# Kernel optimization log

Measured on AMD Instinct MI355X. Metric: run time of the kernel, lower is better.

## Reference

```python
import jax, jax.numpy as jnp
import numpy as np

D_MODEL = 1024
NUM_HEADS = 16
HEAD_DIM = D_MODEL // NUM_HEADS
FFN_HIDDEN = 4096
EPS = 1e-5


def setup_inputs() -> dict:
    key = jax.random.key(0)
    ks = jax.random.split(key, 7)
    s = 0.02
    return {
        "x": jax.random.normal(ks[0], (2, 2048, D_MODEL), dtype=jnp.float32),
        "W_qkv": jax.random.normal(ks[1], (D_MODEL, 3 * D_MODEL), dtype=jnp.float32) * s,
        "b_qkv": jnp.zeros((3 * D_MODEL,), dtype=jnp.float32),
        "W_o": jax.random.normal(ks[2], (D_MODEL, D_MODEL), dtype=jnp.float32) * s,
        "b_o": jnp.zeros((D_MODEL,), dtype=jnp.float32),
        "gamma1": jnp.ones((D_MODEL,), dtype=jnp.float32),
        "beta1": jnp.zeros((D_MODEL,), dtype=jnp.float32),
        "W1": jax.random.normal(ks[3], (D_MODEL, FFN_HIDDEN), dtype=jnp.float32) * s,
        "b1": jnp.zeros((FFN_HIDDEN,), dtype=jnp.float32),
        "W2": jax.random.normal(ks[4], (FFN_HIDDEN, D_MODEL), dtype=jnp.float32) * s,
        "b2": jnp.zeros((D_MODEL,), dtype=jnp.float32),
        "gamma2": jnp.ones((D_MODEL,), dtype=jnp.float32),
        "beta2": jnp.zeros((D_MODEL,), dtype=jnp.float32),
    }


def _layernorm(x, gamma, beta):
    mean = jnp.mean(x, axis=-1, keepdims=True)
    var = jnp.mean((x - mean) ** 2, axis=-1, keepdims=True)
    return gamma * (x - mean) / jnp.sqrt(var + EPS) + beta


def reference(x, W_qkv, b_qkv, W_o, b_o, gamma1, beta1, W1, b1, W2, b2, gamma2, beta2):
    B, S, D = x.shape
    # ---- multi-head attention ----
    qkv = x @ W_qkv + b_qkv                       # [B,S,3D]
    qkv = qkv.reshape(B, S, NUM_HEADS, 3 * HEAD_DIM).transpose(0, 2, 1, 3)  # [B,H,S,3hd]
    q, k, v = jnp.split(qkv, 3, axis=-1)          # each [B,H,S,hd]
    scores = jnp.einsum("bhqd,bhkd->bhqk", q, k) / np.sqrt(HEAD_DIM)
    attn = jax.nn.softmax(scores, axis=-1)
    vals = jnp.einsum("bhqk,bhkd->bhqd", attn, v)
    vals = vals.transpose(0, 2, 1, 3).reshape(B, S, D)
    attn_out = vals @ W_o + b_o
    # dropout disabled (eval mode)
    h = _layernorm(attn_out + x, gamma1, beta1)
    # ---- position-wise FFN (dropout before relu per source, disabled) ----
    ffn = jax.nn.relu(h @ W1 + b1) @ W2 + b2
    return _layernorm(ffn + h, gamma2, beta2)
```

## Files before the change

### kernel.cpp

```cpp
#include <hip/hip_runtime.h>
#include <stdint.h>

typedef float v4f __attribute__((ext_vector_type(4)));
typedef __bf16 v8bf __attribute__((ext_vector_type(8)));
typedef unsigned short v8us __attribute__((ext_vector_type(8)));
typedef unsigned short v4us __attribute__((ext_vector_type(4)));

__device__ __forceinline__ float b2f(unsigned short u) {
    union { float f; uint32_t i; } x; x.i = ((uint32_t)u) << 16; return x.f;
}
__device__ __forceinline__ unsigned short f2b(float f) {
    union { float f; uint32_t u; } x; x.f = f;
    uint32_t r = x.u + 0x7fffu + ((x.u >> 16) & 1u);
    return (unsigned short)(r >> 16);
}

__device__ __forceinline__ void stage16(const unsigned short* g,
                                        unsigned short* lds_base, int lane) {
#if __has_builtin(__builtin_amdgcn_global_load_lds)
    __builtin_amdgcn_global_load_lds(
        (const __attribute__((address_space(1))) void*)g,
        (__attribute__((address_space(3))) void*)lds_base, 16, 0, 0);
#else
    *(v8us*)(lds_base + lane * 8) = *(const v8us*)g;
#endif
}

__global__ __launch_bounds__(256) void convert_f32_bf16(
    const float* __restrict__ src, unsigned short* __restrict__ dst)
{
    int i = (blockIdx.x * 256 + threadIdx.x) * 4;
    float4 v = *(const float4*)&src[i];
    v4us o = {f2b(v.x), f2b(v.y), f2b(v.z), f2b(v.w)};
    *(v4us*)&dst[i] = o;
}

__global__ __launch_bounds__(256) void transpose_to_bt(
    const float* __restrict__ W, unsigned short* __restrict__ WT, int K, int N)
{
    __shared__ unsigned short t[64][65];
    const int kb = blockIdx.y * 64, nb = blockIdx.x * 64;
    const int r = threadIdx.x >> 4, c4 = (threadIdx.x & 15) * 4;
    #pragma unroll
    for (int i = 0; i < 4; ++i) {
        int k = r + i * 16;
        float4 v = *(const float4*)&W[(size_t)(kb + k) * N + nb + c4];
        t[c4 + 0][k] = f2b(v.x);
        t[c4 + 1][k] = f2b(v.y);
        t[c4 + 2][k] = f2b(v.z);
        t[c4 + 3][k] = f2b(v.w);
    }
    __syncthreads();
    #pragma unroll
    for (int i = 0; i < 4; ++i) {
        int n = r + i * 16;
        v4us o = {t[n][c4], t[n][c4 + 1], t[n][c4 + 2], t[n][c4 + 3]};
        *(v4us*)&WT[(size_t)(nb + n) * K + kb + c4] = o;
    }
}

__global__ __launch_bounds__(256) void gemm_bt(
    const unsigned short* __restrict__ A, const unsigned short* __restrict__ BT,
    const float* __restrict__ bias, unsigned short* __restrict__ C,
    int M, int N, int K, int relu)
{
    __shared__ __align__(16) unsigned short sA[2][128 * 32];
    __shared__ __align__(16) unsigned short sB[2][128 * 32];
    const int tid  = threadIdx.x;
    const int wave = tid >> 6, lane = tid & 63;
    const int wm = wave >> 1, wn = wave & 1;
    const int quad = lane >> 4, l16 = lane & 15;
    const int bm = blockIdx.y, bn = blockIdx.x;

    const int srow = lane >> 2, scol = (lane & 3) * 8;
    const unsigned short* ga0 = A  + (size_t)(bm * 128 + (wave * 2 + 0) * 16 + srow) * K + scol;
    const unsigned short* ga1 = A  + (size_t)(bm * 128 + (wave * 2 + 1) * 16 + srow) * K + scol;
    const unsigned short* gb0 = BT + (size_t)(bn * 128 + (wave * 2 + 0) * 16 + srow) * K + scol;
    const unsigned short* gb1 = BT + (size_t)(bn * 128 + (wave * 2 + 1) * 16 + srow) * K + scol;
    const int o0 = (wave * 2 + 0) * 512, o1 = (wave * 2 + 1) * 512;

    v4f acc[4][4];
    #pragma unroll
    for (int i = 0; i < 4; ++i)
        #pragma unroll
        for (int j = 0; j < 4; ++j)
            acc[i][j] = (v4f){0.f, 0.f, 0.f, 0.f};

    for (int kt = 0; kt < K; kt += 64) {
        __syncthreads();
        #pragma unroll
        for (int c = 0; c < 2; ++c) {
            int kc = kt + c * 32;
            stage16(ga0 + kc, &sA[c][o0], lane);
            stage16(ga1 + kc, &sA[c][o1], lane);
            stage16(gb0 + kc, &sB[c][o0], lane);
            stage16(gb1 + kc, &sB[c][o1], lane);
        }
        __syncthreads();

        #pragma unroll
        for (int c = 0; c < 2; ++c) {
            v8bf af[4], bfr[4];
            #pragma unroll
            for (int mt = 0; mt < 4; ++mt)
                af[mt] = *(const v8bf*)&sA[c][(wm * 64 + mt * 16 + l16) * 32 + quad * 8];
            #pragma unroll
            for (int nt = 0; nt < 4; ++nt)
                bfr[nt] = *(const v8bf*)&sB[c][(wn * 64 + nt * 16 + l16) * 32 + quad * 8];
            #pragma unroll
            for (int mt = 0; mt < 4; ++mt)
                #pragma unroll
                for (int nt = 0; nt < 4; ++nt)
                    acc[mt][nt] = __builtin_amdgcn_mfma_f32_16x16x32_bf16(
                        af[mt], bfr[nt], acc[mt][nt], 0, 0, 0);
        }
    }

    #pragma unroll
    for (int mt = 0; mt < 4; ++mt) {
        #pragma unroll
        for (int nt = 0; nt < 4; ++nt) {
            int col = bn * 128 + wn * 64 + nt * 16 + l16;
            float bv = bias ? bias[col] : 0.f;
            #pragma unroll
            for (int r = 0; r < 4; ++r) {
                int row = bm * 128 + wm * 64 + mt * 16 + quad * 4 + r;
                float v = acc[mt][nt][r] + bv;
                if (relu) v = fmaxf(v, 0.f);
                C[(size_t)row * N + col] = f2b(v);
            }
        }
    }
}

__global__ __launch_bounds__(256) void gemm_bt_n64(
    const unsigned short* __restrict__ A, const unsigned short* __restrict__ BT,
    const float* __restrict__ bias, unsigned short* __restrict__ C,
    int M, int N, int K, int relu)
{
    __shared__ __align__(16) unsigned short sA[2][128 * 32];
    __shared__ __align__(16) unsigned short sB[2][64 * 32];
    const int tid  = threadIdx.x;
    const int wave = tid >> 6, lane = tid & 63;
    const int wm = wave >> 1, wn = wave & 1;
    const int quad = lane >> 4, l16 = lane & 15;
    const int bm = blockIdx.y, bn = blockIdx.x;

    const int srow = lane >> 2, scol = (lane & 3) * 8;
    const unsigned short* ga0 = A  + (size_t)(bm * 128 + (wave * 2 + 0) * 16 + srow) * K + scol;
    const unsigned short* ga1 = A  + (size_t)(bm * 128 + (wave * 2 + 1) * 16 + srow) * K + scol;
    const unsigned short* gb0 = BT + (size_t)(bn * 64 + wave * 16 + srow) * K + scol;
    const int oa0 = (wave * 2 + 0) * 512, oa1 = (wave * 2 + 1) * 512, ob = wave * 512;

    v4f acc[4][2];
    #pragma unroll
    for (int i = 0; i < 4; ++i)
        #pragma unroll
        for (int j = 0; j < 2; ++j)
            acc[i][j] = (v4f){0.f, 0.f, 0.f, 0.f};

    for (int kt = 0; kt < K; kt += 64) {
        __syncthreads();
        #pragma unroll
        for (int c = 0; c < 2; ++c) {
            int kc = kt + c * 32;
            stage16(ga0 + kc, &sA[c][oa0], lane);
            stage16(ga1 + kc, &sA[c][oa1], lane);
            stage16(gb0 + kc, &sB[c][ob], lane);
        }
        __syncthreads();

        #pragma unroll
        for (int c = 0; c < 2; ++c) {
            v8bf af[4], bfr[2];
            #pragma unroll
            for (int mt = 0; mt < 4; ++mt)
                af[mt] = *(const v8bf*)&sA[c][(wm * 64 + mt * 16 + l16) * 32 + quad * 8];
            #pragma unroll
            for (int nt = 0; nt < 2; ++nt)
                bfr[nt] = *(const v8bf*)&sB[c][(wn * 32 + nt * 16 + l16) * 32 + quad * 8];
            #pragma unroll
            for (int mt = 0; mt < 4; ++mt)
                #pragma unroll
                for (int nt = 0; nt < 2; ++nt)
                    acc[mt][nt] = __builtin_amdgcn_mfma_f32_16x16x32_bf16(
                        af[mt], bfr[nt], acc[mt][nt], 0, 0, 0);
        }
    }

    #pragma unroll
    for (int mt = 0; mt < 4; ++mt) {
        #pragma unroll
        for (int nt = 0; nt < 2; ++nt) {
            int col = bn * 64 + wn * 32 + nt * 16 + l16;
            float bv = bias ? bias[col] : 0.f;
            #pragma unroll
            for (int r = 0; r < 4; ++r) {
                int row = bm * 128 + wm * 64 + mt * 16 + quad * 4 + r;
                float v = acc[mt][nt][r] + bv;
                if (relu) v = fmaxf(v, 0.f);
                C[(size_t)row * N + col] = f2b(v);
            }
        }
    }
}

__global__ __launch_bounds__(256, 4) void attn_mfma(
    const unsigned short* __restrict__ qkv, unsigned short* __restrict__ av)
{
    __shared__ __align__(16) unsigned short sK[64 * 72];
    __shared__ __align__(16) unsigned short sVT[64 * 72];
    __shared__ __align__(16) unsigned short sP[4][16 * 72];
    const int tid  = threadIdx.x;
    const int wave = tid >> 6, lane = tid & 63;
    const int quad = lane >> 4, l16 = lane & 15;
    const int blk = blockIdx.x;
    const int qb = blk & 31, bh = blk >> 5;
    const int h = bh & 15, b = bh >> 4;
    const int row0 = b * 2048;
    const int qbase = row0 + qb * 64 + wave * 16;
    const size_t qoff = (size_t)h * 192;
    const size_t koff = qoff + 64, voff = qoff + 128;

    v8bf qf[2];
    #pragma unroll
    for (int kc = 0; kc < 2; ++kc)
        qf[kc] = *(const v8bf*)&qkv[(size_t)(qbase + l16) * 3072 + qoff + kc * 32 + quad * 8];

    v4f o[4];
    #pragma unroll
    for (int dt = 0; dt < 4; ++dt) o[dt] = (v4f){0.f, 0.f, 0.f, 0.f};
    float ll = 0.f;

    const float C1 = 0.125f * 1.44269504089f;

    const int k_key0 = tid >> 3,        k_oct = (tid & 7) * 8;
    const int k_key1 = (tid + 256) >> 3;
    const int v_key  = tid & 63;
    const int v_d0   = (tid >> 6) * 8,  v_d1 = v_d0 + 32;
    const unsigned short* gK0 = qkv + (size_t)(row0 + k_key0) * 3072 + koff + k_oct;
    const unsigned short* gK1 = qkv + (size_t)(row0 + k_key1) * 3072 + koff + k_oct;
    const unsigned short* gV0 = qkv + (size_t)(row0 + v_key) * 3072 + voff + v_d0;
    const unsigned short* gV1 = qkv + (size_t)(row0 + v_key) * 3072 + voff + v_d1;
    const size_t step = (size_t)64 * 3072;

    v8us kreg0 = *(const v8us*)gK0, kreg1 = *(const v8us*)gK1;
    v8us vreg0 = *(const v8us*)gV0, vreg1 = *(const v8us*)gV1;
    gK0 += step; gK1 += step; gV0 += step; gV1 += step;

    for (int kt = 0; kt < 32; ++kt) {
        __syncthreads();
        *(v8us*)&sK[k_key0 * 72 + k_oct] = kreg0;
        *(v8us*)&sK[k_key1 * 72 + k_oct] = kreg1;
        #pragma unroll
        for (int j = 0; j < 8; ++j) {
            sVT[(v_d0 + j) * 72 + v_key] = vreg0[j];
            sVT[(v_d1 + j) * 72 + v_key] = vreg1[j];
        }
        __syncthreads();
        if (kt < 31) {
            kreg0 = *(const v8us*)gK0; kreg1 = *(const v8us*)gK1;
            vreg0 = *(const v8us*)gV0; vreg1 = *(const v8us*)gV1;
            gK0 += step; gK1 += step; gV0 += step; gV1 += step;
        }

        v4f sc[4];
        #pragma unroll
        for (int kk = 0; kk < 4; ++kk) {
            sc[kk] = (v4f){0.f, 0.f, 0.f, 0.f};
            #pragma unroll
            for (int kc = 0; kc < 2; ++kc) {
                v8bf ak = *(const v8bf*)&sK[(kk * 16 + l16) * 72 + kc * 32 + quad * 8];
                sc[kk] = __builtin_amdgcn_mfma_f32_16x16x32_bf16(ak, qf[kc], sc[kk], 0, 0, 0);
            }
        }

        float ps = 0.f;
        #pragma unroll
        for (int kk = 0; kk < 4; ++kk) {
            v4us pk;
            #pragma unroll
            for (int rr = 0; rr < 4; ++rr) {
                float p = __builtin_amdgcn_exp2f(sc[kk][rr] * C1);
                ps += p;
                pk[rr] = f2b(p);
            }
            *(v4us*)&sP[wave][l16 * 72 + kk * 16 + quad * 4] = pk;
        }
        ll += ps;

        __asm__ volatile("s_waitcnt lgkmcnt(0)" ::: "memory");

        #pragma unroll
        for (int c = 0; c < 2; ++c) {
            v8bf pb;
            {
                union { v8bf v; v8us u; } u;
                u.u = *(const v8us*)&sP[wave][l16 * 72 + c * 32 + quad * 8];
                pb = u.v;
            }
            #pragma unroll
            for (int dt = 0; dt < 4; ++dt) {
                v8bf va = *(const v8bf*)&sVT[(dt * 16 + l16) * 72 + c * 32 + quad * 8];
                o[dt] = __builtin_amdgcn_mfma_f32_16x16x32_bf16(va, pb, o[dt], 0, 0, 0);
            }
        }
    }

    ll += __shfl_xor(ll, 16, 64);
    ll += __shfl_xor(ll, 32, 64);
    float inv = 1.f / ll;
    int qrow = qbase + l16;
    #pragma unroll
    for (int dt = 0; dt < 4; ++dt) {
        v4us st;
        #pragma unroll
        for (int rr = 0; rr < 4; ++rr)
            st[rr] = f2b(o[dt][rr] * inv);
        *(v4us*)&av[(size_t)qrow * 1024 + h * 64 + dt * 16 + quad * 4] = st;
    }
}

template<int RES_F32, int OUT_F32>
__global__ __launch_bounds__(256) void ln_fused(
    const unsigned short* __restrict__ a, const void* __restrict__ residv,
    const float* __restrict__ gamma, const float* __restrict__ beta,
    void* __restrict__ outv)
{
    const int row = blockIdx.x, tid = threadIdx.x;
    const size_t base = (size_t)row * 1024;
    const int c0 = tid * 4;
    ushort4 avv = *(const ushort4*)&a[base + c0];
    float y[4];
    if (RES_F32) {
        float4 rv = *(const float4*)((const float*)residv + base + c0);
        y[0] = b2f(avv.x) + rv.x;
        y[1] = b2f(avv.y) + rv.y;
        y[2] = b2f(avv.z) + rv.z;
        y[3] = b2f(avv.w) + rv.w;
    } else {
        ushort4 rv = *(const ushort4*)((const unsigned short*)residv + base + c0);
        y[0] = b2f(avv.x) + b2f(rv.x);
        y[1] = b2f(avv.y) + b2f(rv.y);
        y[2] = b2f(avv.z) + b2f(rv.z);
        y[3] = b2f(avv.w) + b2f(rv.w);
    }
    float s  = y[0] + y[1] + y[2] + y[3];
    float ss = y[0]*y[0] + y[1]*y[1] + y[2]*y[2] + y[3]*y[3];
    #pragma unroll
    for (int off = 32; off; off >>= 1) {
        s  += __shfl_xor(s, off, 64);
        ss += __shfl_xor(ss, off, 64);
    }
    __shared__ float red[8];
    int wave = tid >> 6, lane = tid & 63;
    if (lane == 0) { red[wave] = s; red[4 + wave] = ss; }
    __syncthreads();
    s  = red[0] + red[1] + red[2] + red[3];
    ss = red[4] + red[5] + red[6] + red[7];
    float mean = s * (1.f / 1024.f);
    float var  = ss * (1.f / 1024.f) - mean * mean;
    float rstd = rsqrtf(var + 1e-5f);
    float4 gv = *(const float4*)&gamma[c0];
    float4 bv = *(const float4*)&beta[c0];
    float r0 = gv.x * (y[0] - mean) * rstd + bv.x;
    float r1 = gv.y * (y[1] - mean) * rstd + bv.y;
    float r2 = gv.z * (y[2] - mean) * rstd + bv.z;
    float r3 = gv.w * (y[3] - mean) * rstd + bv.w;
    if (OUT_F32) {
        float4 ov = {r0, r1, r2, r3};
        *(float4*)((float*)outv + base + c0) = ov;
    } else {
        ushort4 ov;
        ov.x = f2b(r0); ov.y = f2b(r1); ov.z = f2b(r2); ov.w = f2b(r3);
        *(ushort4*)((unsigned short*)outv + base + c0) = ov;
    }
}

extern "C" void kernel_launch(void* const* d_in, const int* in_sizes, int n_in,
                              void* d_out, int out_size, void* d_ws, size_t ws_size,
                              hipStream_t stream)
{
    (void)in_sizes; (void)n_in; (void)out_size; (void)ws_size;
    const float* x    = (const float*)d_in[0];
    const float* Wqkv = (const float*)d_in[1];
    const float* bqkv = (const float*)d_in[2];
    const float* Wo   = (const float*)d_in[3];
    const float* bo   = (const float*)d_in[4];
    const float* g1   = (const float*)d_in[5];
    const float* be1  = (const float*)d_in[6];
    const float* W1   = (const float*)d_in[7];
    const float* b1   = (const float*)d_in[8];
    const float* W2   = (const float*)d_in[9];
    const float* b2   = (const float*)d_in[10];
    const float* g2   = (const float*)d_in[11];
    const float* be2  = (const float*)d_in[12];
    float* out = (float*)d_out;

    unsigned short* R0 = (unsigned short*)d_ws;
    unsigned short* R1 = R0 + (size_t)16 * 1024 * 1024;
    unsigned short* R2 = R1 + (size_t)4 * 1024 * 1024;
    unsigned short* R3 = R2 + (size_t)4 * 1024 * 1024;
    unsigned short* WqkvT = R0 + (size_t)12 * 1024 * 1024;

    const int M = 4096;
    dim3 blk(256);

    convert_f32_bf16<<<dim3(M * 1024 / 1024), blk, 0, stream>>>(x, R2);
    transpose_to_bt<<<dim3(48, 16), blk, 0, stream>>>(Wqkv, WqkvT, 1024, 3072);
    gemm_bt<<<dim3(24, 32), blk, 0, stream>>>(R2, WqkvT, bqkv, R0, M, 3072, 1024, 0);
    attn_mfma<<<dim3(1024), blk, 0, stream>>>(R0, R1);
    transpose_to_bt<<<dim3(16, 16), blk, 0, stream>>>(Wo, R2, 1024, 1024);
    gemm_bt_n64<<<dim3(16, 32), blk, 0, stream>>>(R1, R2, bo, R3, M, 1024, 1024, 0);
    ln_fused<1, 0><<<dim3(4096), blk, 0, stream>>>(R3, x, g1, be1, R2);
    transpose_to_bt<<<dim3(64, 16), blk, 0, stream>>>(W1, R1, 1024, 4096);
    gemm_bt<<<dim3(32, 32), blk, 0, stream>>>(R2, R1, b1, R0, M, 4096, 1024, 1);
    transpose_to_bt<<<dim3(16, 64), blk, 0, stream>>>(W2, R3, 4096, 1024);
    gemm_bt_n64<<<dim3(16, 32), blk, 0, stream>>>(R0, R3, b2, R1, M, 1024, 4096, 0);
    ln_fused<0, 1><<<dim3(4096), blk, 0, stream>>>(R1, R2, g2, be2, out);
}
```

Before: 391.8 us.

## Write V transposed from the QKV GEMM epilogue to avoid scalar LDS transposes

The QKV GEMM epilogue now writes the V columns straight into a per-head transposed buffer [b,h,d,s], so the attention kernel can stage V^T with vector 16-byte LDS stores instead of 16 scalar strided stores per thread. Workspace buffers are reshuffled to make room for the new VT region. The bf16 conversions in attention also switch to native __bf16 casts. The risk is that the 8-byte strided VT stores in the GEMM epilogue are poorly coalesced, and the extra branch adds cost to that epilogue.

Result: faster. 383.6 us (-2.1%).

```diff
diff --git a/kernel.cpp b/kernel.cpp
--- a/kernel.cpp
+++ b/kernel.cpp
@@ -3,6 +3,7 @@
 
 typedef float v4f __attribute__((ext_vector_type(4)));
 typedef __bf16 v8bf __attribute__((ext_vector_type(8)));
+typedef __bf16 v4bf __attribute__((ext_vector_type(4)));
 typedef unsigned short v8us __attribute__((ext_vector_type(8)));
 typedef unsigned short v4us __attribute__((ext_vector_type(4)));
 
@@ -59,10 +60,11 @@
     }
 }
 
+template<int SPLIT_V>
 __global__ __launch_bounds__(256) void gemm_bt(
     const unsigned short* __restrict__ A, const unsigned short* __restrict__ BT,
     const float* __restrict__ bias, unsigned short* __restrict__ C,
-    int M, int N, int K, int relu)
+    unsigned short* __restrict__ VT, int M, int N, int K, int relu)
 {
     __shared__ __align__(16) unsigned short sA[2][128 * 32];
     __shared__ __align__(16) unsigned short sB[2][128 * 32];
@@ -118,16 +120,29 @@
 
     #pragma unroll
     for (int mt = 0; mt < 4; ++mt) {
+        int row = bm * 128 + wm * 64 + mt * 16 + quad * 4;
         #pragma unroll
         for (int nt = 0; nt < 4; ++nt) {
-            int col = bn * 128 + wn * 64 + nt * 16 + l16;
+            int c0 = bn * 128 + wn * 64 + nt * 16;
+            int col = c0 + l16;
             float bv = bias ? bias[col] : 0.f;
-            #pragma unroll
-            for (int r = 0; r < 4; ++r) {
-                int row = bm * 128 + wm * 64 + mt * 16 + quad * 4 + r;
-                float v = acc[mt][nt][r] + bv;
-                if (relu) v = fmaxf(v, 0.f);
-                C[(size_t)row * N + col] = f2b(v);
+            if (SPLIT_V && (c0 % 192) >= 128) {
+                int hh = c0 / 192;
+                int d  = (c0 % 192) - 128 + l16;
+                int bb = row >> 11;
+                int s  = row & 2047;
+                v4us st;
+                #pragma unroll
+                for (int r = 0; r < 4; ++r)
+                    st[r] = f2b(acc[mt][nt][r] + bv);
+                *(v4us*)&VT[((size_t)(bb * 16 + hh) * 64 + d) * 2048 + s] = st;
+            } else {
+                #pragma unroll
+                for (int r = 0; r < 4; ++r) {
+                    float v = acc[mt][nt][r] + bv;
+                    if (relu) v = fmaxf(v, 0.f);
+                    C[(size_t)(row + r) * N + col] = f2b(v);
+                }
             }
         }
     }
@@ -206,7 +221,8 @@
 }
 
 __global__ __launch_bounds__(256, 4) void attn_mfma(
-    const unsigned short* __restrict__ qkv, unsigned short* __restrict__ av)
+    const unsigned short* __restrict__ qkv, const unsigned short* __restrict__ VT,
+    unsigned short* __restrict__ av)
 {
     __shared__ __align__(16) unsigned short sK[64 * 72];
     __shared__ __align__(16) unsigned short sVT[64 * 72];
@@ -220,7 +236,7 @@
     const int row0 = b * 2048;
     const int qbase = row0 + qb * 64 + wave * 16;
     const size_t qoff = (size_t)h * 192;
-    const size_t koff = qoff + 64, voff = qoff + 128;
+    const size_t koff = qoff + 64;
 
     v8bf qf[2];
     #pragma unroll
@@ -236,32 +252,30 @@
 
     const int k_key0 = tid >> 3,        k_oct = (tid & 7) * 8;
     const int k_key1 = (tid + 256) >> 3;
-    const int v_key  = tid & 63;
-    const int v_d0   = (tid >> 6) * 8,  v_d1 = v_d0 + 32;
+    const int v_d0 = tid >> 3,          v_koct = (tid & 7) * 8;
+    const int v_d1 = (tid + 256) >> 3;
     const unsigned short* gK0 = qkv + (size_t)(row0 + k_key0) * 3072 + koff + k_oct;
     const unsigned short* gK1 = qkv + (size_t)(row0 + k_key1) * 3072 + koff + k_oct;
-    const unsigned short* gV0 = qkv + (size_t)(row0 + v_key) * 3072 + voff + v_d0;
-    const unsigned short* gV1 = qkv + (size_t)(row0 + v_key) * 3072 + voff + v_d1;
-    const size_t step = (size_t)64 * 3072;
+    const unsigned short* gV0 = VT + ((size_t)bh * 64 + v_d0) * 2048 + v_koct;
+    const unsigned short* gV1 = VT + ((size_t)bh * 64 + v_d1) * 2048 + v_koct;
+    const size_t stepK = (size_t)64 * 3072;
+    const size_t stepV = 64;
 
     v8us kreg0 = *(const v8us*)gK0, kreg1 = *(const v8us*)gK1;
     v8us vreg0 = *(const v8us*)gV0, vreg1 = *(const v8us*)gV1;
-    gK0 += step; gK1 += step; gV0 += step; gV1 += step;
+    gK0 += stepK; gK1 += stepK; gV0 += stepV; gV1 += stepV;
 
     for (int kt = 0; kt < 32; ++kt) {
         __syncthreads();
         *(v8us*)&sK[k_key0 * 72 + k_oct] = kreg0;
         *(v8us*)&sK[k_key1 * 72 + k_oct] = kreg1;
-        #pragma unroll
-        for (int j = 0; j < 8; ++j) {
-            sVT[(v_d0 + j) * 72 + v_key] = vreg0[j];
-            sVT[(v_d1 + j) * 72 + v_key] = vreg1[j];
-        }
+        *(v8us*)&sVT[v_d0 * 72 + v_koct] = vreg0;
+        *(v8us*)&sVT[v_d1 * 72 + v_koct] = vreg1;
         __syncthreads();
         if (kt < 31) {
             kreg0 = *(const v8us*)gK0; kreg1 = *(const v8us*)gK1;
             vreg0 = *(const v8us*)gV0; vreg1 = *(const v8us*)gV1;
-            gK0 += step; gK1 += step; gV0 += step; gV1 += step;
+            gK0 += stepK; gK1 += stepK; gV0 += stepV; gV1 += stepV;
         }
 
         v4f sc[4];
@@ -278,14 +292,14 @@
         float ps = 0.f;
         #pragma unroll
         for (int kk = 0; kk < 4; ++kk) {
-            v4us pk;
+            v4bf pk;
             #pragma unroll
             for (int rr = 0; rr < 4; ++rr) {
                 float p = __builtin_amdgcn_exp2f(sc[kk][rr] * C1);
                 ps += p;
-                pk[rr] = f2b(p);
-            }
-            *(v4us*)&sP[wave][l16 * 72 + kk * 16 + quad * 4] = pk;
+                pk[rr] = (__bf16)p;
+            }
+            *(v4bf*)&sP[wave][l16 * 72 + kk * 16 + quad * 4] = pk;
         }
         ll += ps;
 
@@ -313,11 +327,11 @@
     int qrow = qbase + l16;
     #pragma unroll
     for (int dt = 0; dt < 4; ++dt) {
-        v4us st;
+        v4bf st;
         #pragma unroll
         for (int rr = 0; rr < 4; ++rr)
-            st[rr] = f2b(o[dt][rr] * inv);
-        *(v4us*)&av[(size_t)qrow * 1024 + h * 64 + dt * 16 + quad * 4] = st;
+            st[rr] = (__bf16)(o[dt][rr] * inv);
+        *(v4bf*)&av[(size_t)qrow * 1024 + h * 64 + dt * 16 + quad * 4] = st;
     }
 }
 
@@ -408,14 +422,14 @@
 
     convert_f32_bf16<<<dim3(M * 1024 / 1024), blk, 0, stream>>>(x, R2);
     transpose_to_bt<<<dim3(48, 16), blk, 0, stream>>>(Wqkv, WqkvT, 1024, 3072);
-    gemm_bt<<<dim3(24, 32), blk, 0, stream>>>(R2, WqkvT, bqkv, R0, M, 3072, 1024, 0);
-    attn_mfma<<<dim3(1024), blk, 0, stream>>>(R0, R1);
+    gemm_bt<1><<<dim3(24, 32), blk, 0, stream>>>(R2, WqkvT, bqkv, R0, R1, M, 3072, 1024, 0);
+    attn_mfma<<<dim3(1024), blk, 0, stream>>>(R0, R1, R3);
     transpose_to_bt<<<dim3(16, 16), blk, 0, stream>>>(Wo, R2, 1024, 1024);
-    gemm_bt_n64<<<dim3(16, 32), blk, 0, stream>>>(R1, R2, bo, R3, M, 1024, 1024, 0);
-    ln_fused<1, 0><<<dim3(4096), blk, 0, stream>>>(R3, x, g1, be1, R2);
-    transpose_to_bt<<<dim3(64, 16), blk, 0, stream>>>(W1, R1, 1024, 4096);
-    gemm_bt<<<dim3(32, 32), blk, 0, stream>>>(R2, R1, b1, R0, M, 4096, 1024, 1);
-    transpose_to_bt<<<dim3(16, 64), blk, 0, stream>>>(W2, R3, 4096, 1024);
-    gemm_bt_n64<<<dim3(16, 32), blk, 0, stream>>>(R0, R3, b2, R1, M, 1024, 4096, 0);
-    ln_fused<0, 1><<<dim3(4096), blk, 0, stream>>>(R1, R2, g2, be2, out);
-}
+    gemm_bt_n64<<<dim3(16, 32), blk, 0, stream>>>(R3, R2, bo, R1, M, 1024, 1024, 0);
+    ln_fused<1, 0><<<dim3(4096), blk, 0, stream>>>(R1, x, g1, be1, R2);
+    transpose_to_bt<<<dim3(64, 16), blk, 0, stream>>>(W1, R3, 1024, 4096);
+    gemm_bt<0><<<dim3(32, 32), blk, 0, stream>>>(R2, R3, b1, R0, nullptr, M, 4096, 1024, 1);
+    transpose_to_bt<<<dim3(16, 64), blk, 0, stream>>>(W2, R1, 4096, 1024);
+    gemm_bt_n64<<<dim3(16, 32), blk, 0, stream>>>(R0, R1, b2, R3, M, 1024, 4096, 0);
+    ln_fused<0, 1><<<dim3(4096), blk, 0, stream>>>(R3, R2, g2, be2, out);
+}
```
